# Kernel tuning notes

Measured on AMD Instinct MI355X. Metric: run time of the kernel, lower is better.

Reference implementation:

```python
import jax, jax.numpy as jnp
import numpy as np

BETA = 0.95
THRESHOLD = 1.0
NUM_STEPS = 25


def setup_inputs() -> dict:
    key = jax.random.key(0)
    ks = jax.random.split(key, 5)
    B, NIN, NH, NOUT = 16384, 784, 500, 10
    # Kaiming-uniform-ish scales like nn.Linear defaults
    s1 = 1.0 / np.sqrt(NIN)
    s2 = 1.0 / np.sqrt(NH)
    return {
        "x": jax.random.uniform(ks[0], (B, NIN), dtype=jnp.float32),
        "w1": jax.random.normal(ks[1], (NH, NIN), dtype=jnp.float32) * s1,
        "b1": jax.random.normal(ks[2], (NH,), dtype=jnp.float32) * s1,
        "w2": jax.random.normal(ks[3], (NOUT, NH), dtype=jnp.float32) * s2,
        "b2": jax.random.normal(ks[4], (NOUT,), dtype=jnp.float32) * s2,
    }


def _heaviside(x):
    return (x > 0).astype(x.dtype)


def reference(x, w1, b1, w2, b2):
    B = x.shape[0]
    NH = w1.shape[0]
    NOUT = w2.shape[0]
    # cur1 is identical every step (x is static) but we keep it inside the
    # scan body to mirror the original per-step fc1(x) computation.
    def step(carry, _):
        mem1, mem2 = carry
        cur1 = x @ w1.T + b1                      # [B, 500]
        # snntorch Leaky, reset_mechanism='subtract':
        # reset from PREVIOUS mem (detached), spike from NEW mem
        reset1 = jax.lax.stop_gradient(_heaviside(mem1 - THRESHOLD))
        mem1 = BETA * mem1 + cur1 - reset1 * THRESHOLD
        spk1 = _heaviside(mem1 - THRESHOLD)
        cur2 = spk1 @ w2.T + b2                   # [B, 10]
        reset2 = jax.lax.stop_gradient(_heaviside(mem2 - THRESHOLD))
        mem2 = BETA * mem2 + cur2 - reset2 * THRESHOLD
        spk2 = _heaviside(mem2 - THRESHOLD)
        return (mem1, mem2), (spk2, mem2)

    init = (jnp.zeros((B, NH), x.dtype), jnp.zeros((B, NOUT), x.dtype))
    _, (spk2_rec, mem2_rec) = jax.lax.scan(step, init, None, length=NUM_STEPS)
    return spk2_rec, mem2_rec  # each [25, B, 10]
```

## Files before the change

### kernel.cpp

```cpp
#include <hip/hip_runtime.h>
#include <stdint.h>

#define B_ROWS 16384
#define NIN    784
#define NH     500
#define NHP    512
#define NOUT   10
#define STEPS  25


__global__ __launch_bounds__(256) void k0_wtrans(
    const float* __restrict__ w1, float* __restrict__ w1tb)
{
    const int i  = blockIdx.x * 256 + threadIdx.x;
    const int u  = i & 511;
    const int kb = i >> 9;
    if (kb >= 196) return;
    float4 v = make_float4(0.f, 0.f, 0.f, 0.f);
    if (u < NH) v = *(const float4*)(w1 + (size_t)u * NIN + kb * 4);
    *(float4*)(w1tb + (size_t)kb * 2048 + u * 4) = v;
}


#define K1_R 16

__global__ __launch_bounds__(256) void k1_fc1(
    const float* __restrict__ x, const float* __restrict__ w1tb,
    const float* __restrict__ b1, uint32_t* __restrict__ masks_g)
{
    const int t    = threadIdx.x;
    const int row0 = blockIdx.x * K1_R;

    float accA[2][K1_R], accB[2][K1_R];
#pragma unroll
    for (int u = 0; u < 2; ++u)
#pragma unroll
        for (int r = 0; r < K1_R; ++r) { accA[u][r] = 0.f; accB[u][r] = 0.f; }

    for (int kb = 0; kb < 128; ++kb) {
        const float4 wv0 = *(const float4*)(w1tb + (size_t)kb * 2048 + t * 4);
        const float4 wv1 = *(const float4*)(w1tb + (size_t)kb * 2048 + (t + 256) * 4);
#pragma unroll
        for (int r = 0; r < K1_R; ++r) {
            const float* xr = x + (size_t)(row0 + r) * NIN + kb * 4;
            const float x0 = xr[0], x1 = xr[1], x2 = xr[2], x3 = xr[3];
            accA[0][r] = fmaf(x0, wv0.x, accA[0][r]);
            accA[0][r] = fmaf(x1, wv0.y, accA[0][r]);
            accA[0][r] = fmaf(x2, wv0.z, accA[0][r]);
            accA[0][r] = fmaf(x3, wv0.w, accA[0][r]);
            accA[1][r] = fmaf(x0, wv1.x, accA[1][r]);
            accA[1][r] = fmaf(x1, wv1.y, accA[1][r]);
            accA[1][r] = fmaf(x2, wv1.z, accA[1][r]);
            accA[1][r] = fmaf(x3, wv1.w, accA[1][r]);
        }
    }
    for (int kb = 128; kb < 196; ++kb) {
        const float4 wv0 = *(const float4*)(w1tb + (size_t)kb * 2048 + t * 4);
        const float4 wv1 = *(const float4*)(w1tb + (size_t)kb * 2048 + (t + 256) * 4);
#pragma unroll
        for (int r = 0; r < K1_R; ++r) {
            const float* xr = x + (size_t)(row0 + r) * NIN + kb * 4;
            const float x0 = xr[0], x1 = xr[1], x2 = xr[2], x3 = xr[3];
            accB[0][r] = fmaf(x0, wv0.x, accB[0][r]);
            accB[0][r] = fmaf(x1, wv0.y, accB[0][r]);
            accB[0][r] = fmaf(x2, wv0.z, accB[0][r]);
            accB[0][r] = fmaf(x3, wv0.w, accB[0][r]);
            accB[1][r] = fmaf(x0, wv1.x, accB[1][r]);
            accB[1][r] = fmaf(x1, wv1.y, accB[1][r]);
            accB[1][r] = fmaf(x2, wv1.z, accB[1][r]);
            accB[1][r] = fmaf(x3, wv1.w, accB[1][r]);
        }
    }

#pragma unroll
    for (int uu = 0; uu < 2; ++uu) {
        const int u = t + uu * 256;
        if (u >= NH) continue;
        const float bb = b1[u];
#pragma unroll
        for (int r = 0; r < K1_R; ++r) {
            const float dot = __fadd_rn(accA[uu][r], accB[uu][r]);
            const float c   = __fadd_rn(dot, bb);
            float m = 0.f;
            uint32_t bits = 0;
#pragma unroll
            for (int st = 0; st < STEPS; ++st) {
                const float rs = (m > 1.0f) ? 1.0f : 0.0f;
                m = __fsub_rn(__fadd_rn(__fmul_rn(0.95f, m), c), rs);
                bits |= ((m > 1.0f) ? 1u : 0u) << st;
            }
            masks_g[(size_t)(row0 + r) * NHP + u] = bits;
        }
    }
}


#define K2_RPB 10

__global__ __launch_bounds__(256) void k2_fc2(
    const uint32_t* __restrict__ masks_g, const float* __restrict__ w2,
    const float* __restrict__ b2, float* __restrict__ out)
{
    __shared__ float w2s[NH][NOUT];
    __shared__ float b2s[NOUT];
    __shared__ float c2[K2_RPB][NOUT][STEPS + 1];

    const int t    = threadIdx.x;
    const int row0 = blockIdx.x * K2_RPB;

    for (int i = t; i < NH * NOUT; i += 256) {
        const int h = i / NOUT, o = i - h * NOUT;
        w2s[h][o] = w2[o * NH + h];
    }
    if (t < NOUT) b2s[t] = b2[t];
    __syncthreads();

    const int rl = t / STEPS;
    const int st = t - rl * STEPS;
    const int row = row0 + rl;

    if (t < K2_RPB * STEPS && row < B_ROWS) {
        float a[NOUT];
#pragma unroll
        for (int o = 0; o < NOUT; ++o) a[o] = 0.f;
        const uint32_t* mrow = masks_g + (size_t)row * NHP;
        for (int h = 0; h < NH; ++h) {
            const float s = (float)((mrow[h] >> st) & 1u);
#pragma unroll
            for (int o = 0; o < NOUT; ++o)
                a[o] = fmaf(s, w2s[h][o], a[o]);
        }
#pragma unroll
        for (int o = 0; o < NOUT; ++o) c2[rl][o][st] = a[o];
    }
    __syncthreads();

    if (t < K2_RPB * NOUT) {
        const int r2 = t / NOUT, o = t - r2 * NOUT;
        const int row2 = row0 + r2;
        if (row2 < B_ROWS) {
            float* spk_out = out;
            float* mem_out = out + (size_t)STEPS * B_ROWS * NOUT;
            const size_t base = (size_t)row2 * NOUT + o;
            const float bo = b2s[o];
            float m = 0.f;
#pragma unroll
            for (int s2 = 0; s2 < STEPS; ++s2) {
                const float c  = __fadd_rn(c2[r2][o][s2], bo);
                const float rs = (m > 1.0f) ? 1.0f : 0.0f;
                m = __fsub_rn(__fadd_rn(__fmul_rn(0.95f, m), c), rs);
                const size_t idx = (size_t)s2 * (B_ROWS * NOUT) + base;
                spk_out[idx] = (m > 1.0f) ? 1.0f : 0.0f;
                mem_out[idx] = m;
            }
        }
    }
}

extern "C" void kernel_launch(void* const* d_in, const int* in_sizes, int n_in,
                              void* d_out, int out_size, void* d_ws, size_t ws_size,
                              hipStream_t stream)
{
    const float* x  = (const float*)d_in[0];
    const float* w1 = (const float*)d_in[1];
    const float* b1 = (const float*)d_in[2];
    const float* w2 = (const float*)d_in[3];
    const float* b2 = (const float*)d_in[4];
    float* out = (float*)d_out;

    float*    w1tb    = (float*)d_ws;
    uint32_t* masks_g = (uint32_t*)((char*)d_ws + 1605632);

    k0_wtrans<<<dim3(392), 256, 0, stream>>>(w1, w1tb);
    k1_fc1<<<dim3(B_ROWS / K1_R), 256, 0, stream>>>(x, w1tb, b1, masks_g);
    k2_fc2<<<dim3((B_ROWS + K2_RPB - 1) / K2_RPB), 256, 0, stream>>>(masks_g, w2, b2, out);
}
```

Measured before the change: 326.3 us.

## Stage x rows in LDS, prefetch weights, process two row tiles per block

The fc1 kernel now loads each block's 16 input rows into shared memory with coalesced float4 loads and reads them from LDS as float4, instead of issuing scalar global loads that are uniform across the wavefront. Weight vectors are software-prefetched one k-block ahead. Each block processes two row tiles, which halves the grid. The fc2 kernel reads the mask row as uint4 vectors. The aim is to cut global load instructions and latency, at the cost of 50KB of LDS per block, which may limit occupancy.

```diff
diff --git a/kernel.cpp b/kernel.cpp
--- a/kernel.cpp
+++ b/kernel.cpp
@@ -28,68 +28,87 @@
     const float* __restrict__ x, const float* __restrict__ w1tb,
     const float* __restrict__ b1, uint32_t* __restrict__ masks_g)
 {
-    const int t    = threadIdx.x;
-    const int row0 = blockIdx.x * K1_R;
-
-    float accA[2][K1_R], accB[2][K1_R];
-#pragma unroll
-    for (int u = 0; u < 2; ++u)
-#pragma unroll
-        for (int r = 0; r < K1_R; ++r) { accA[u][r] = 0.f; accB[u][r] = 0.f; }
-
-    for (int kb = 0; kb < 128; ++kb) {
-        const float4 wv0 = *(const float4*)(w1tb + (size_t)kb * 2048 + t * 4);
-        const float4 wv1 = *(const float4*)(w1tb + (size_t)kb * 2048 + (t + 256) * 4);
-#pragma unroll
-        for (int r = 0; r < K1_R; ++r) {
-            const float* xr = x + (size_t)(row0 + r) * NIN + kb * 4;
-            const float x0 = xr[0], x1 = xr[1], x2 = xr[2], x3 = xr[3];
-            accA[0][r] = fmaf(x0, wv0.x, accA[0][r]);
-            accA[0][r] = fmaf(x1, wv0.y, accA[0][r]);
-            accA[0][r] = fmaf(x2, wv0.z, accA[0][r]);
-            accA[0][r] = fmaf(x3, wv0.w, accA[0][r]);
-            accA[1][r] = fmaf(x0, wv1.x, accA[1][r]);
-            accA[1][r] = fmaf(x1, wv1.y, accA[1][r]);
-            accA[1][r] = fmaf(x2, wv1.z, accA[1][r]);
-            accA[1][r] = fmaf(x3, wv1.w, accA[1][r]);
-        }
-    }
-    for (int kb = 128; kb < 196; ++kb) {
-        const float4 wv0 = *(const float4*)(w1tb + (size_t)kb * 2048 + t * 4);
-        const float4 wv1 = *(const float4*)(w1tb + (size_t)kb * 2048 + (t + 256) * 4);
-#pragma unroll
-        for (int r = 0; r < K1_R; ++r) {
-            const float* xr = x + (size_t)(row0 + r) * NIN + kb * 4;
-            const float x0 = xr[0], x1 = xr[1], x2 = xr[2], x3 = xr[3];
-            accB[0][r] = fmaf(x0, wv0.x, accB[0][r]);
-            accB[0][r] = fmaf(x1, wv0.y, accB[0][r]);
-            accB[0][r] = fmaf(x2, wv0.z, accB[0][r]);
-            accB[0][r] = fmaf(x3, wv0.w, accB[0][r]);
-            accB[1][r] = fmaf(x0, wv1.x, accB[1][r]);
-            accB[1][r] = fmaf(x1, wv1.y, accB[1][r]);
-            accB[1][r] = fmaf(x2, wv1.z, accB[1][r]);
-            accB[1][r] = fmaf(x3, wv1.w, accB[1][r]);
-        }
-    }
-
-#pragma unroll
-    for (int uu = 0; uu < 2; ++uu) {
-        const int u = t + uu * 256;
-        if (u >= NH) continue;
-        const float bb = b1[u];
-#pragma unroll
-        for (int r = 0; r < K1_R; ++r) {
-            const float dot = __fadd_rn(accA[uu][r], accB[uu][r]);
-            const float c   = __fadd_rn(dot, bb);
-            float m = 0.f;
-            uint32_t bits = 0;
-#pragma unroll
-            for (int st = 0; st < STEPS; ++st) {
-                const float rs = (m > 1.0f) ? 1.0f : 0.0f;
-                m = __fsub_rn(__fadd_rn(__fmul_rn(0.95f, m), c), rs);
-                bits |= ((m > 1.0f) ? 1u : 0u) << st;
-            }
-            masks_g[(size_t)(row0 + r) * NHP + u] = bits;
+    __shared__ alignas(16) float xs[K1_R][NIN];
+    const int t = threadIdx.x;
+
+    for (int tile = 0; tile < 2; ++tile) {
+        const int row0 = (blockIdx.x * 2 + tile) * K1_R;
+
+        __syncthreads();
+        for (int i = t; i < K1_R * (NIN / 4); i += 256) {
+            const int r = i / (NIN / 4), q = i - r * (NIN / 4);
+            *(float4*)&xs[r][q * 4] =
+                *(const float4*)(x + (size_t)(row0 + r) * NIN + q * 4);
+        }
+        __syncthreads();
+
+        float accA[2][K1_R], accB[2][K1_R];
+#pragma unroll
+        for (int u = 0; u < 2; ++u)
+#pragma unroll
+            for (int r = 0; r < K1_R; ++r) { accA[u][r] = 0.f; accB[u][r] = 0.f; }
+
+        float4 wc0 = *(const float4*)(w1tb + (size_t)0 * 2048 + t * 4);
+        float4 wc1 = *(const float4*)(w1tb + (size_t)0 * 2048 + (t + 256) * 4);
+
+        for (int kb = 0; kb < 128; ++kb) {
+            const float4 wn0 = *(const float4*)(w1tb + (size_t)(kb + 1) * 2048 + t * 4);
+            const float4 wn1 = *(const float4*)(w1tb + (size_t)(kb + 1) * 2048 + (t + 256) * 4);
+#pragma unroll
+            for (int r = 0; r < K1_R; ++r) {
+                const float4 xv = *(const float4*)&xs[r][kb * 4];
+                accA[0][r] = fmaf(xv.x, wc0.x, accA[0][r]);
+                accA[0][r] = fmaf(xv.y, wc0.y, accA[0][r]);
+                accA[0][r] = fmaf(xv.z, wc0.z, accA[0][r]);
+                accA[0][r] = fmaf(xv.w, wc0.w, accA[0][r]);
+                accA[1][r] = fmaf(xv.x, wc1.x, accA[1][r]);
+                accA[1][r] = fmaf(xv.y, wc1.y, accA[1][r]);
+                accA[1][r] = fmaf(xv.z, wc1.z, accA[1][r]);
+                accA[1][r] = fmaf(xv.w, wc1.w, accA[1][r]);
+            }
+            wc0 = wn0; wc1 = wn1;
+        }
+        for (int kb = 128; kb < 196; ++kb) {
+            float4 wn0, wn1;
+            const bool pf = (kb < 195);
+            if (pf) {
+                wn0 = *(const float4*)(w1tb + (size_t)(kb + 1) * 2048 + t * 4);
+                wn1 = *(const float4*)(w1tb + (size_t)(kb + 1) * 2048 + (t + 256) * 4);
+            }
+#pragma unroll
+            for (int r = 0; r < K1_R; ++r) {
+                const float4 xv = *(const float4*)&xs[r][kb * 4];
+                accB[0][r] = fmaf(xv.x, wc0.x, accB[0][r]);
+                accB[0][r] = fmaf(xv.y, wc0.y, accB[0][r]);
+                accB[0][r] = fmaf(xv.z, wc0.z, accB[0][r]);
+                accB[0][r] = fmaf(xv.w, wc0.w, accB[0][r]);
+                accB[1][r] = fmaf(xv.x, wc1.x, accB[1][r]);
+                accB[1][r] = fmaf(xv.y, wc1.y, accB[1][r]);
+                accB[1][r] = fmaf(xv.z, wc1.z, accB[1][r]);
+                accB[1][r] = fmaf(xv.w, wc1.w, accB[1][r]);
+            }
+            if (pf) { wc0 = wn0; wc1 = wn1; }
+        }
+
+#pragma unroll
+        for (int uu = 0; uu < 2; ++uu) {
+            const int u = t + uu * 256;
+            if (u >= NH) continue;
+            const float bb = b1[u];
+#pragma unroll
+            for (int r = 0; r < K1_R; ++r) {
+                const float dot = __fadd_rn(accA[uu][r], accB[uu][r]);
+                const float c   = __fadd_rn(dot, bb);
+                float m = 0.f;
+                uint32_t bits = 0;
+#pragma unroll
+                for (int st = 0; st < STEPS; ++st) {
+                    const float rs = (m > 1.0f) ? 1.0f : 0.0f;
+                    m = __fsub_rn(__fadd_rn(__fmul_rn(0.95f, m), c), rs);
+                    bits |= ((m > 1.0f) ? 1u : 0u) << st;
+                }
+                masks_g[(size_t)(row0 + r) * NHP + u] = bits;
+            }
         }
     }
 }
@@ -123,12 +142,18 @@
         float a[NOUT];
 #pragma unroll
         for (int o = 0; o < NOUT; ++o) a[o] = 0.f;
-        const uint32_t* mrow = masks_g + (size_t)row * NHP;
-        for (int h = 0; h < NH; ++h) {
-            const float s = (float)((mrow[h] >> st) & 1u);
-#pragma unroll
-            for (int o = 0; o < NOUT; ++o)
-                a[o] = fmaf(s, w2s[h][o], a[o]);
+        const uint4* m4 = (const uint4*)(masks_g + (size_t)row * NHP);
+        for (int hq = 0; hq < NH / 4; ++hq) {
+            const uint4 q = m4[hq];
+            const uint32_t mw[4] = {q.x, q.y, q.z, q.w};
+#pragma unroll
+            for (int cc = 0; cc < 4; ++cc) {
+                const float s = (float)((mw[cc] >> st) & 1u);
+                const float* wp = &w2s[4 * hq + cc][0];
+#pragma unroll
+                for (int o = 0; o < NOUT; ++o)
+                    a[o] = fmaf(s, wp[o], a[o]);
+            }
         }
 #pragma unroll
         for (int o = 0; o < NOUT; ++o) c2[rl][o][st] = a[o];
@@ -172,6 +197,6 @@
     uint32_t* masks_g = (uint32_t*)((char*)d_ws + 1605632);
 
     k0_wtrans<<<dim3(392), 256, 0, stream>>>(w1, w1tb);
-    k1_fc1<<<dim3(B_ROWS / K1_R), 256, 0, stream>>>(x, w1tb, b1, masks_g);
+    k1_fc1<<<dim3(B_ROWS / (K1_R * 2)), 256, 0, stream>>>(x, w1tb, b1, masks_g);
     k2_fc2<<<dim3((B_ROWS + K2_RPB - 1) / K2_RPB), 256, 0, stream>>>(masks_g, w2, b2, out);
 }
```

After: 343.6 us. +5.3%, slower.
